# Kernel tuning notes

Measured on AMD Instinct MI355X. Metric: run time of the kernel, lower is better.

Reference implementation:

```python
import jax, jax.numpy as jnp
import numpy as np

NUM_LAYERS = 6
D_MODEL = 768
N_HEADS = 8
D_QKV = D_MODEL // N_HEADS
D_FF = 3072
OUT_DIM = 80
MAX_REL = 100  # relative_positional_distance
NUM_REL = 2 * MAX_REL + 1
LN_EPS = 1e-5


def layer_norm(x, g, b):
    mu = jnp.mean(x, axis=-1, keepdims=True)
    var = jnp.mean((x - mu) ** 2, axis=-1, keepdims=True)
    return (x - mu) / jnp.sqrt(var + LN_EPS) * g + b


def rel_positional_logits(q, emb):
    # q: (B,H,L,dq) (already scaled by 1/sqrt(dq)); emb: (H, 2*MAX_REL+1, dq)
    B, H, L, dq = q.shape
    pad_len = max(L - MAX_REL, 0)
    start = max(MAX_REL - L, 0)
    padded = jnp.pad(emb, ((0, 0), (pad_len, pad_len), (0, 0)))
    used = padded[:, start:start + 2 * L - 1]  # (H, 2L-1, dq)
    logits = jnp.einsum('bhld,hmd->bhlm', q, used)  # (B,H,L,2L-1)
    if L > MAX_REL:
        # mask unreachable relative positions (|rel| beyond table) with -1e8
        mask = jnp.zeros((2 * L - 1,), logits.dtype)
        mask = mask.at[:pad_len].set(-1e8).at[-pad_len:].set(-1e8)
        logits = logits + mask
    # relative -> absolute indexing (fairseq skew trick)
    x = jnp.pad(logits, ((0, 0), (0, 0), (0, 0), (0, 1)))       # (B,H,L,2L)
    x = x.reshape(B, H, L * 2 * L)
    x = jnp.pad(x, ((0, 0), (0, 0), (0, L - 1)))
    x = x.reshape(B, H, L + 1, 2 * L - 1)
    return x[:, :, :L, L - 1:]  # (B,H,L,L)


def self_attention(x, wq, wk, wv, wo, emb):
    # x: (T,B,D); wq/wk/wv: (H,D,dq); wo: (H,dq,D); emb: (H,NUM_REL,dq)
    q = jnp.einsum('tbf,hfa->bhta', x, wq) / (D_QKV ** 0.5)
    k = jnp.einsum('tbf,hfa->bhta', x, wk)
    v = jnp.einsum('tbf,hfa->bhta', x, wv)
    logits = jnp.einsum('bhqa,bhka->bhqk', q, k) + rel_positional_logits(q, emb)
    probs = jax.nn.softmax(logits, axis=-1)
    o = jnp.einsum('bhqk,bhka->bhqa', probs, v)
    return jnp.einsum('bhta,had->tbd', o, wo)


def forward(x, wq, wk, wv, wo, rel_emb, ff1_w, ff1_b, ff2_w, ff2_b,
            ln1_g, ln1_b, ln2_g, ln2_b, wout, bout):
    # x: (B,T,D)
    src = jnp.transpose(x, (1, 0, 2))  # (T,B,D)
    for l in range(NUM_LAYERS):
        attn = self_attention(src, wq[l], wk[l], wv[l], wo[l], rel_emb[l])
        src = layer_norm(src + attn, ln1_g[l], ln1_b[l])
        h = jax.nn.relu(src @ ff1_w[l].T + ff1_b[l])
        ff = h @ ff2_w[l].T + ff2_b[l]
        src = layer_norm(src + ff, ln2_g[l], ln2_b[l])
    out = jnp.transpose(src, (1, 0, 2))  # (B,T,D)
    return out @ wout.T + bout


def setup_inputs() -> dict:
    key = jax.random.key(0)
    ks = jax.random.split(key, 17)
    B, T = 8, 512
    s_d = 1.0 / np.sqrt(D_MODEL)
    s_q = 1.0 / np.sqrt(D_QKV)
    s_f = 1.0 / np.sqrt(D_FF)
    f32 = jnp.float32
    return {
        'x': jax.random.normal(ks[0], (B, T, D_MODEL), f32),
        'wq': jax.random.normal(ks[1], (NUM_LAYERS, N_HEADS, D_MODEL, D_QKV), f32) * s_d,
        'wk': jax.random.normal(ks[2], (NUM_LAYERS, N_HEADS, D_MODEL, D_QKV), f32) * s_d,
        'wv': jax.random.normal(ks[3], (NUM_LAYERS, N_HEADS, D_MODEL, D_QKV), f32) * s_d,
        'wo': jax.random.normal(ks[4], (NUM_LAYERS, N_HEADS, D_QKV, D_MODEL), f32) * s_q,
        'rel_emb': jax.random.normal(ks[5], (NUM_LAYERS, N_HEADS, NUM_REL, D_QKV), f32) * s_q,
        'ff1_w': jax.random.normal(ks[6], (NUM_LAYERS, D_FF, D_MODEL), f32) * s_d,
        'ff1_b': jnp.zeros((NUM_LAYERS, D_FF), f32),
        'ff2_w': jax.random.normal(ks[7], (NUM_LAYERS, D_MODEL, D_FF), f32) * s_f,
        'ff2_b': jnp.zeros((NUM_LAYERS, D_MODEL), f32),
        'ln1_g': jnp.ones((NUM_LAYERS, D_MODEL), f32),
        'ln1_b': jnp.zeros((NUM_LAYERS, D_MODEL), f32),
        'ln2_g': jnp.ones((NUM_LAYERS, D_MODEL), f32),
        'ln2_b': jnp.zeros((NUM_LAYERS, D_MODEL), f32),
        'wout': jax.random.normal(ks[8], (OUT_DIM, D_MODEL), f32) * s_d,
        'bout': jnp.zeros((OUT_DIM,), f32),
    }


def reference(x, wq, wk, wv, wo, rel_emb, ff1_w, ff1_b, ff2_w, ff2_b,
              ln1_g, ln1_b, ln2_g, ln2_b, wout, bout):
    return forward(x, wq, wk, wv, wo, rel_emb, ff1_w, ff1_b, ff2_w, ff2_b,
                   ln1_g, ln1_b, ln2_g, ln2_b, wout, bout)
```

## Files before the change

### kernel.cpp

```cpp
#include <hip/hip_runtime.h>
#include <hip/hip_bf16.h>
#include <math.h>

#define NL   6
#define DM   768
#define NH   8
#define DQ   96
#define DFF  3072
#define BB   8
#define TT   512
#define NTOK (BB*TT)
#define NREL 201
#define WIN  99
#define ODIM 80
#define NQKV 2304
#define RELD 208

typedef __attribute__((ext_vector_type(8))) short v8s;
typedef __attribute__((ext_vector_type(4))) float v4f;

static __device__ __forceinline__ short bf16bits(float x) {
  __hip_bfloat16 h = __float2bfloat16(x);
  return *(short*)&h;
}
static __device__ __forceinline__ unsigned short bf16u(float x) {
  __hip_bfloat16 h = __float2bfloat16(x);
  return *(unsigned short*)&h;
}

__global__ void k_transpose_in(const float* __restrict__ x, float* __restrict__ src,
                               __hip_bfloat16* __restrict__ srcb) {
  int n = blockIdx.x;
  int t = n >> 3, b = n & 7;
  const float* xi = x + ((size_t)b*TT + t)*DM;
  for (int d = threadIdx.x; d < DM; d += blockDim.x) {
    float v = xi[d];
    src[(size_t)n*DM + d] = v;
    srcb[(size_t)n*DM + d] = __float2bfloat16(v);
  }
}

__global__ __launch_bounds__(256)
void k_conv_qkvw(const float* __restrict__ wq, const float* __restrict__ wk,
                 const float* __restrict__ wv, __hip_bfloat16* __restrict__ o) {
  __shared__ float tile[64][33];
  const int ft = blockIdx.x, at = blockIdx.y;
  const int l = blockIdx.z >> 3, h = blockIdx.z & 7;
  const int f0 = ft*64, a0 = at*32;
  const int tx = threadIdx.x & 31, ty = threadIdx.x >> 5;
  const float* srcs[3] = {wq, wk, wv};
  #pragma unroll
  for (int part = 0; part < 3; ++part) {
    const float* s = srcs[part] + (size_t)l*DM*DM + (size_t)h*DM*DQ;
    #pragma unroll
    for (int p = 0; p < 8; ++p)
      tile[ty + 8*p][tx] = s[(size_t)(f0 + ty + 8*p)*DQ + (a0 + tx)];
    __syncthreads();
    const float sc = (part == 0) ? 0.10206207261596577f : 1.f;
    unsigned short* d = (unsigned short*)o + (size_t)l*NQKV*DM + (size_t)(part*DM + h*DQ)*DM;
    #pragma unroll
    for (int p = 0; p < 4; ++p) {
      int a = ty + 8*p;
      int f = 2*tx;
      ushort2 pr = make_ushort2(bf16u(tile[f][a]*sc), bf16u(tile[f+1][a]*sc));
      *(ushort2*)(d + (size_t)(a0 + a)*DM + f0 + f) = pr;
    }
    __syncthreads();
  }
}

__global__ __launch_bounds__(256)
void k_conv_wo(const float* __restrict__ wo, __hip_bfloat16* __restrict__ o) {
  __shared__ float tile[64][33];
  const int rt = blockIdx.x, dt = blockIdx.y, l = blockIdx.z;
  const int r0 = rt*64, d0 = dt*32;
  const int tx = threadIdx.x & 31, ty = threadIdx.x >> 5;
  const float* s = wo + (size_t)l*DM*DM;
  #pragma unroll
  for (int p = 0; p < 8; ++p)
    tile[ty + 8*p][tx] = s[(size_t)(r0 + ty + 8*p)*DM + d0 + tx];
  __syncthreads();
  unsigned short* d = (unsigned short*)o + (size_t)l*DM*DM;
  #pragma unroll
  for (int p = 0; p < 4; ++p) {
    int dd = ty + 8*p;
    int r = 2*tx;
    ushort2 pr = make_ushort2(bf16u(tile[r][dd]), bf16u(tile[r+1][dd]));
    *(ushort2*)(d + (size_t)(d0 + dd)*DM + r0 + r) = pr;
  }
}

__global__ void k_cast(const float* __restrict__ in, __hip_bfloat16* __restrict__ o, size_t n) {
  size_t idx = (size_t)blockIdx.x*256 + threadIdx.x;
  if (idx < n) o[idx] = __float2bfloat16(in[idx]);
}

__global__ void k_conv_wout(const float* __restrict__ wout, __hip_bfloat16* __restrict__ o) {
  int idx = blockIdx.x*256 + threadIdx.x;
  if (idx >= 128*DM) return;
  int n = idx / DM, f = idx % DM;
  o[idx] = __float2bfloat16(n < ODIM ? wout[(size_t)n*DM + f] : 0.f);
}

template<int BM, int BN, int WM, int WN, bool DBUF, bool RELU, bool BF16OUT, bool PERM>
__global__ __launch_bounds__(256)
void k_mfma_gemm(const __hip_bfloat16* __restrict__ A, const __hip_bfloat16* __restrict__ Bt,
                 const float* __restrict__ bias, void* __restrict__ Cv,
                 int K, int Nvalid, int ldc) {
  constexpr int NWN = BN/WN;
  constexpr int FM = WM/16, FN = WN/16;
  constexpr int NB = DBUF ? 2 : 1;
  __shared__ __align__(16) short As[NB][BM*64];
  __shared__ __align__(16) short Bs[NB][BN*64];
  const int tid = threadIdx.x;
  const int m0 = blockIdx.x*BM, n0 = blockIdx.y*BN;
  const int lane = tid & 63, w = tid >> 6;
  const int wm = (w / NWN)*WM, wn = (w % NWN)*WN;
  const int mr = lane & 15, q4 = lane >> 4;
  const short* Ag = (const short*)A;
  const short* Bg = (const short*)Bt;
  const v4f zero = {0.f, 0.f, 0.f, 0.f};
  v4f acc[FM][FN];
  #pragma unroll
  for (int i=0;i<FM;++i)
    #pragma unroll
    for (int j=0;j<FN;++j) acc[i][j] = zero;

  auto stage = [&](int k0, int buf) {
    #pragma unroll
    for (int s = 0; s < (BM*8)/256; ++s) {
      int cid = s*256 + tid;
      int row = cid >> 3;
      int c = (cid & 7) ^ (row & 7);
      __builtin_amdgcn_global_load_lds(
        (const __attribute__((address_space(1))) void*)(Ag + (size_t)(m0+row)*K + k0 + c*8),
        (__attribute__((address_space(3))) void*)(&As[buf][cid*8]), 16, 0, 0);
    }
    #pragma unroll
    for (int s = 0; s < (BN*8)/256; ++s) {
      int cid = s*256 + tid;
      int row = cid >> 3;
      int c = (cid & 7) ^ (row & 7);
      __builtin_amdgcn_global_load_lds(
        (const __attribute__((address_space(1))) void*)(Bg + (size_t)(n0+row)*K + k0 + c*8),
        (__attribute__((address_space(3))) void*)(&Bs[buf][cid*8]), 16, 0, 0);
    }
  };

  auto compute = [&](const short* Ab, const short* Bb) {
    #pragma unroll
    for (int kh = 0; kh < 2; ++kh) {
      int pos = (kh*4 + q4) ^ (mr & 7);
      v8s af[FM], bf[FN];
      #pragma unroll
      for (int ii=0;ii<FM;++ii) af[ii] = *(const v8s*)(Ab + (wm + ii*16 + mr)*64 + pos*8);
      #pragma unroll
      for (int j=0;j<FN;++j) bf[j] = *(const v8s*)(Bb + (wn + j*16 + mr)*64 + pos*8);
      #pragma unroll
      for (int ii=0;ii<FM;++ii)
        #pragma unroll
        for (int j=0;j<FN;++j)
          acc[ii][j] = __builtin_amdgcn_mfma_f32_16x16x32_bf16(af[ii], bf[j], acc[ii][j], 0, 0, 0);
    }
  };

  const int nk = K >> 6;
  if (DBUF) {
    stage(0, 0);
    for (int i = 0; i < nk; ++i) {
      __syncthreads();
      if (i + 1 < nk) stage((i+1)*64, (i+1)&1);
      compute(As[i&1], Bs[i&1]);
    }
  } else {
    for (int i = 0; i < nk; ++i) {
      stage(i*64, 0);
      __syncthreads();
      compute(As[0], Bs[0]);
      __syncthreads();
    }
  }

  #pragma unroll
  for (int j=0;j<FN;++j) {
    int col = n0 + wn + j*16 + mr;
    if (col < Nvalid) {
      float bv = bias ? bias[col] : 0.f;
      #pragma unroll
      for (int i=0;i<FM;++i) {
        #pragma unroll
        for (int r=0;r<4;++r) {
          int m = m0 + wm + i*16 + q4*4 + r;
          float val = acc[i][j][r] + bv;
          if (RELU) val = fmaxf(val, 0.f);
          int row = PERM ? ((m & 7)*TT + (m >> 3)) : m;
          if (BF16OUT) ((__hip_bfloat16*)Cv)[(size_t)row*ldc + col] = __float2bfloat16(val);
          else         ((float*)Cv)[(size_t)row*ldc + col] = val;
        }
      }
    }
  }
}

__global__ __launch_bounds__(256)
void k_rel_gemm(const __hip_bfloat16* __restrict__ qkvb,
                const __hip_bfloat16* __restrict__ embb,
                float* __restrict__ rel) {
  const int e0 = blockIdx.x*64, m0 = blockIdx.y*64, h = blockIdx.z;
  const int tid = threadIdx.x, lane = tid & 63, w = tid >> 6;
  const int l15 = lane & 15, q4 = lane >> 4;
  __shared__ __align__(16) short As[64*104];
  __shared__ __align__(16) short Bs[64*104];
  const short* qg = (const short*)qkvb;
  const short* eg = (const short*)embb;
  {
    int row = tid >> 2;
    const short* sa = qg + (size_t)(m0+row)*NQKV + h*DQ;
    int er = e0 + row; if (er > 200) er = 200;
    const short* sb = eg + ((size_t)h*NREL + er)*DQ;
    short* da = As + row*104;
    short* db = Bs + row*104;
    #pragma unroll
    for (int c = 0; c < 3; ++c) {
      int ch = (tid & 3)*3 + c;
      *(v8s*)(da + ch*8) = *(const v8s*)(sa + ch*8);
      *(v8s*)(db + ch*8) = *(const v8s*)(sb + ch*8);
    }
  }
  __syncthreads();
  const v4f zero = {0.f,0.f,0.f,0.f};
  v4f acc[4] = {zero, zero, zero, zero};
  #pragma unroll
  for (int ks = 0; ks < 3; ++ks) {
    v8s af = *(const v8s*)(As + (w*16 + l15)*104 + ks*32 + q4*8);
    #pragma unroll
    for (int f = 0; f < 4; ++f) {
      v8s bf = *(const v8s*)(Bs + (f*16 + l15)*104 + ks*32 + q4*8);
      acc[f] = __builtin_amdgcn_mfma_f32_16x16x32_bf16(af, bf, acc[f], 0, 0, 0);
    }
  }
  #pragma unroll
  for (int f = 0; f < 4; ++f) {
    int e = e0 + f*16 + l15;
    if (e < 2*WIN + 1) {
      #pragma unroll
      for (int r = 0; r < 4; ++r) {
        int n = m0 + w*16 + q4*4 + r;
        rel[((size_t)h*NTOK + n)*RELD + e] = acc[f][r];
      }
    }
  }
}

__global__ __launch_bounds__(256)
void k_attn_mfma(const __hip_bfloat16* __restrict__ qkvb,
                 const float* __restrict__ rel,
                 __hip_bfloat16* __restrict__ o) {
  const int qt = blockIdx.x, h = blockIdx.y, b = blockIdx.z;
  const int qlo = qt*64;
  const int tid = threadIdx.x, lane = tid & 63, w = tid >> 6;
  const int l15 = lane & 15, q4 = lane >> 4;
  __shared__ __align__(16) short Qs[64*104];
  __shared__ __align__(16) short Ks[64*104];
  __shared__ __align__(16) short Vt[96*72];
  __shared__ __align__(16) short Ps[64*72];
  const short* qg = (const short*)qkvb;

  {
    int row = tid >> 2;
    const short* src = qg + (size_t)((qlo+row)*8 + b)*NQKV + h*DQ;
    short* dst = Qs + row*104;
    #pragma unroll
    for (int c = 0; c < 3; ++c) {
      int ch = (tid & 3)*3 + c;
      *(v8s*)(dst + ch*8) = *(const v8s*)(src + ch*8);
    }
  }

  v4f sacc[5][4];
  const v4f neg = {-1e30f,-1e30f,-1e30f,-1e30f};
  #pragma unroll
  for (int kt=0;kt<5;++kt)
    #pragma unroll
    for (int f=0;f<4;++f) sacc[kt][f] = neg;

  const int i_row0 = qlo + w*16 + q4*4;

  for (int kt = 0; kt < 5; ++kt) {
    int kt0 = qlo + kt*64 - 128;
    if (kt0 + 64 <= 0 || kt0 >= TT) continue;
    {
      int row = tid >> 2;
      int j = kt0 + row; j = j < 0 ? 0 : (j > TT-1 ? TT-1 : j);
      const short* src = qg + (size_t)(j*8 + b)*NQKV + DM + h*DQ;
      short* dst = Ks + row*104;
      #pragma unroll
      for (int c = 0; c < 3; ++c) {
        int ch = (tid & 3)*3 + c;
        *(v8s*)(dst + ch*8) = *(const v8s*)(src + ch*8);
      }
    }
    __syncthreads();
    #pragma unroll
    for (int f = 0; f < 4; ++f) {
      int j = kt0 + f*16 + l15;
      #pragma unroll
      for (int r = 0; r < 4; ++r) {
        int i = i_row0 + r;
        int d = j - i;
        float val = -1e30f;
        if (j >= 0 && j < TT && d >= -WIN && d <= WIN)
          val = rel[((size_t)h*NTOK + i*8 + b)*RELD + d + WIN];
        sacc[kt][f][r] = val;
      }
    }
    #pragma unroll
    for (int ks = 0; ks < 3; ++ks) {
      v8s af = *(const v8s*)(Qs + (w*16 + l15)*104 + ks*32 + q4*8);
      #pragma unroll
      for (int f = 0; f < 4; ++f) {
        v8s bf = *(const v8s*)(Ks + (f*16 + l15)*104 + ks*32 + q4*8);
        sacc[kt][f] = __builtin_amdgcn_mfma_f32_16x16x32_bf16(af, bf, sacc[kt][f], 0, 0, 0);
      }
    }
    __syncthreads();
  }

  float inv[4];
  #pragma unroll
  for (int r = 0; r < 4; ++r) {
    float m = -1e30f;
    #pragma unroll
    for (int kt=0;kt<5;++kt)
      #pragma unroll
      for (int f=0;f<4;++f) m = fmaxf(m, sacc[kt][f][r]);
    #pragma unroll
    for (int off=1; off<16; off<<=1) m = fmaxf(m, __shfl_xor(m, off));
    float l = 0.f;
    #pragma unroll
    for (int kt=0;kt<5;++kt)
      #pragma unroll
      for (int f=0;f<4;++f) {
        float p = __expf(sacc[kt][f][r] - m);
        sacc[kt][f][r] = p; l += p;
      }
    #pragma unroll
    for (int off=1; off<16; off<<=1) l += __shfl_xor(l, off);
    inv[r] = 1.f / l;
  }

  v4f oacc[6];
  const v4f zero = {0.f,0.f,0.f,0.f};
  #pragma unroll
  for (int f=0;f<6;++f) oacc[f] = zero;
  for (int kt = 0; kt < 5; ++kt) {
    int kt0 = qlo + kt*64 - 128;
    if (kt0 + 64 <= 0 || kt0 >= TT) continue;
    #pragma unroll
    for (int f=0;f<4;++f)
      #pragma unroll
      for (int r=0;r<4;++r)
        Ps[(w*16 + q4*4 + r)*72 + f*16 + l15] = bf16bits(sacc[kt][f][r]);
    {
      int j = kt0 + (tid >> 2);
      int jc = j < 0 ? 0 : (j > TT-1 ? TT-1 : j);
      const short* src = qg + (size_t)(jc*8 + b)*NQKV + 2*DM + h*DQ + (tid & 3)*24;
      union { v8s v[3]; short s[24]; } u;
      u.v[0] = *(const v8s*)(src);
      u.v[1] = *(const v8s*)(src + 8);
      u.v[2] = *(const v8s*)(src + 16);
      int a0 = (tid & 3)*24, jl = tid >> 2;
      #pragma unroll
      for (int t=0;t<24;++t) Vt[(a0+t)*72 + jl] = u.s[t];
    }
    __syncthreads();
    #pragma unroll
    for (int ks=0;ks<2;++ks) {
      v8s af = *(const v8s*)(Ps + (w*16 + l15)*72 + ks*32 + q4*8);
      #pragma unroll
      for (int f=0;f<6;++f) {
        v8s bf = *(const v8s*)(Vt + (f*16 + l15)*72 + ks*32 + q4*8);
        oacc[f] = __builtin_amdgcn_mfma_f32_16x16x32_bf16(af, bf, oacc[f], 0, 0, 0);
      }
    }
    __syncthreads();
  }

  #pragma unroll
  for (int f=0;f<6;++f)
    #pragma unroll
    for (int r=0;r<4;++r) {
      int i = i_row0 + r;
      o[(size_t)(i*8 + b)*DM + h*DQ + f*16 + l15] = __float2bfloat16(oacc[f][r] * inv[r]);
    }
}

__global__ __launch_bounds__(256)
void k_ln_residual(float* __restrict__ src, const float* __restrict__ res,
                   const float* __restrict__ g, const float* __restrict__ bta,
                   __hip_bfloat16* __restrict__ srcb) {
  __shared__ float red[4];
  int n = blockIdx.x;
  float x[3];
  float s = 0.f;
  #pragma unroll
  for (int u=0;u<3;++u) {
    int d = u*256 + threadIdx.x;
    x[u] = src[(size_t)n*DM + d] + res[(size_t)n*DM + d];
    s += x[u];
  }
  #pragma unroll
  for (int off=32; off; off>>=1) s += __shfl_xor(s, off);
  if ((threadIdx.x & 63) == 0) red[threadIdx.x>>6] = s;
  __syncthreads();
  float mu = (red[0]+red[1]+red[2]+red[3]) * (1.f/DM);
  __syncthreads();
  float vs = 0.f;
  #pragma unroll
  for (int u=0;u<3;++u) { float dv = x[u]-mu; vs += dv*dv; }
  #pragma unroll
  for (int off=32; off; off>>=1) vs += __shfl_xor(vs, off);
  if ((threadIdx.x & 63) == 0) red[threadIdx.x>>6] = vs;
  __syncthreads();
  float rstd = rsqrtf((red[0]+red[1]+red[2]+red[3])*(1.f/DM) + 1e-5f);
  #pragma unroll
  for (int u=0;u<3;++u) {
    int d = u*256 + threadIdx.x;
    float v = (x[u]-mu)*rstd*g[d] + bta[d];
    src[(size_t)n*DM + d] = v;
    srcb[(size_t)n*DM + d] = __float2bfloat16(v);
  }
}

extern "C" void kernel_launch(void* const* d_in, const int* in_sizes, int n_in,
                              void* d_out, int out_size, void* d_ws, size_t ws_size,
                              hipStream_t stream) {
  const float* x    = (const float*)d_in[0];
  const float* wq   = (const float*)d_in[1];
  const float* wk   = (const float*)d_in[2];
  const float* wv   = (const float*)d_in[3];
  const float* wo   = (const float*)d_in[4];
  const float* remb = (const float*)d_in[5];
  const float* ff1w = (const float*)d_in[6];
  const float* ff1b = (const float*)d_in[7];
  const float* ff2w = (const float*)d_in[8];
  const float* ff2b = (const float*)d_in[9];
  const float* ln1g = (const float*)d_in[10];
  const float* ln1b = (const float*)d_in[11];
  const float* ln2g = (const float*)d_in[12];
  const float* ln2b = (const float*)d_in[13];
  const float* wout = (const float*)d_in[14];
  const float* bout = (const float*)d_in[15];
  float* out = (float*)d_out;

  float* wsp = (float*)d_ws;
  size_t off = 0;
  float* src  = wsp + off;                              off += (size_t)NTOK*DM;
  __hip_bfloat16* srcb  = (__hip_bfloat16*)(wsp + off); off += (size_t)NTOK*DM/2;
  __hip_bfloat16* qkvb  = (__hip_bfloat16*)(wsp + off); off += (size_t)NTOK*NQKV/2;
  float* rel  = wsp + off;                              off += (size_t)NH*NTOK*RELD;
  float* tmp  = wsp + off;                              off += (size_t)NTOK*DM;
  __hip_bfloat16* qkvwbA = (__hip_bfloat16*)(wsp + off); off += (size_t)NL*NQKV*DM/2;
  __hip_bfloat16* wobA   = (__hip_bfloat16*)(wsp + off); off += (size_t)NL*DM*DM/2;
  __hip_bfloat16* ff1wbA = (__hip_bfloat16*)(wsp + off); off += (size_t)NL*DFF*DM/2;
  __hip_bfloat16* ff2wbA = (__hip_bfloat16*)(wsp + off); off += (size_t)NL*DM*DFF/2;
  __hip_bfloat16* woutb  = (__hip_bfloat16*)(wsp + off); off += (size_t)128*DM/2;
  __hip_bfloat16* embbA  = (__hip_bfloat16*)(wsp + off); off += (size_t)NL*NH*NREL*DQ/2 + 64;
  __hip_bfloat16* hb  = (__hip_bfloat16*)qkvb;
  __hip_bfloat16* obb = srcb;
  (void)off; (void)ws_size; (void)in_sizes; (void)n_in; (void)out_size;

  dim3 b256(256);

  k_conv_qkvw<<<dim3(DM/64, DQ/32, NL*NH), b256, 0, stream>>>(wq, wk, wv, qkvwbA);
  k_conv_wo<<<dim3(DM/64, DM/32, NL), b256, 0, stream>>>(wo, wobA);
  k_cast<<<dim3(((size_t)NL*DFF*DM+255)/256), b256, 0, stream>>>(ff1w, ff1wbA, (size_t)NL*DFF*DM);
  k_cast<<<dim3(((size_t)NL*DM*DFF+255)/256), b256, 0, stream>>>(ff2w, ff2wbA, (size_t)NL*DM*DFF);
  k_cast<<<dim3(((size_t)NL*NH*NREL*DQ+255)/256), b256, 0, stream>>>(remb, embbA, (size_t)NL*NH*NREL*DQ);
  k_conv_wout<<<dim3((128*DM+255)/256), b256, 0, stream>>>(wout, woutb);

  k_transpose_in<<<dim3(NTOK), b256, 0, stream>>>(x, src, srcb);

  for (int l = 0; l < NL; ++l) {
    __hip_bfloat16* qkvwb = qkvwbA + (size_t)l*NQKV*DM;
    __hip_bfloat16* wob   = wobA   + (size_t)l*DM*DM;
    __hip_bfloat16* ff1wb = ff1wbA + (size_t)l*DFF*DM;
    __hip_bfloat16* ff2wb = ff2wbA + (size_t)l*DM*DFF;
    __hip_bfloat16* embb  = embbA  + (size_t)l*NH*NREL*DQ;

    k_mfma_gemm<128,128,64,64,false,false,true,false><<<dim3(NTOK/128, NQKV/128), b256, 0, stream>>>(
        srcb, qkvwb, nullptr, qkvb, DM, NQKV, NQKV);

    k_rel_gemm<<<dim3(4, NTOK/64, NH), b256, 0, stream>>>(qkvb, embb, rel);

    k_attn_mfma<<<dim3(TT/64, NH, BB), b256, 0, stream>>>(qkvb, rel, obb);

    k_mfma_gemm<64,64,32,32,true,false,false,false><<<dim3(NTOK/64, DM/64), b256, 0, stream>>>(
        obb, wob, nullptr, tmp, DM, DM, DM);
    k_ln_residual<<<dim3(NTOK), b256, 0, stream>>>(src, tmp, ln1g + (size_t)l*DM, ln1b + (size_t)l*DM, srcb);

    k_mfma_gemm<128,128,64,64,false,true,true,false><<<dim3(NTOK/128, DFF/128), b256, 0, stream>>>(
        srcb, ff1wb, ff1b + (size_t)l*DFF, hb, DM, DFF, DFF);
    k_mfma_gemm<64,64,32,32,true,false,false,false><<<dim3(NTOK/64, DM/64), b256, 0, stream>>>(
        hb, ff2wb, ff2b + (size_t)l*DM, tmp, DFF, DM, DM);
    k_ln_residual<<<dim3(NTOK), b256, 0, stream>>>(src, tmp, ln2g + (size_t)l*DM, ln2b + (size_t)l*DM, srcb);
  }

  k_mfma_gemm<64,128,64,32,true,false,false,true><<<dim3(NTOK/64, 1), b256, 0, stream>>>(
      srcb, woutb, bout, out, DM, ODIM, ODIM);
}
```

Before: 1.147 ms.

## Use 32x32x16 MFMA GEMM with double buffering for all layer projections

Adds a new GEMM kernel built on the 32x32x16 bf16 MFMA instruction, with double-buffered LDS staging. It is used for the QKV, output-projection, FF1 and FF2 GEMMs. Double buffering becomes unconditional in the existing 16x16 kernel, which now serves only the final output projection. The FF2 tile changes to 128x64. The larger MFMA shape is meant to cut LDS fragment loads per flop and improve MFMA throughput, at the cost of more accumulator registers and LDS per block, which may lower occupancy.

```diff
diff --git a/kernel.cpp b/kernel.cpp
--- a/kernel.cpp
+++ b/kernel.cpp
@@ -18,6 +18,7 @@
 
 typedef __attribute__((ext_vector_type(8))) short v8s;
 typedef __attribute__((ext_vector_type(4))) float v4f;
+typedef __attribute__((ext_vector_type(16))) float v16f;
 
 static __device__ __forceinline__ short bf16bits(float x) {
   __hip_bfloat16 h = __float2bfloat16(x);
@@ -102,16 +103,106 @@
   o[idx] = __float2bfloat16(n < ODIM ? wout[(size_t)n*DM + f] : 0.f);
 }
 
-template<int BM, int BN, int WM, int WN, bool DBUF, bool RELU, bool BF16OUT, bool PERM>
+template<int BM, int BN, int WM, int WN, bool RELU, bool BF16OUT>
+__global__ __launch_bounds__(256)
+void k_gemm32(const __hip_bfloat16* __restrict__ A, const __hip_bfloat16* __restrict__ Bt,
+              const float* __restrict__ bias, void* __restrict__ Cv,
+              int K, int ldc) {
+  constexpr int NWN = BN/WN;
+  constexpr int FM = WM/32, FN = WN/32;
+  __shared__ __align__(16) short As[2][BM*64];
+  __shared__ __align__(16) short Bs[2][BN*64];
+  const int tid = threadIdx.x;
+  const int m0 = blockIdx.x*BM, n0 = blockIdx.y*BN;
+  const int lane = tid & 63, w = tid >> 6;
+  const int wm = (w / NWN)*WM, wn = (w % NWN)*WN;
+  const int r31 = lane & 31, h = lane >> 5;
+  const short* Ag = (const short*)A;
+  const short* Bg = (const short*)Bt;
+  v16f acc[FM][FN];
+  #pragma unroll
+  for (int i=0;i<FM;++i)
+    #pragma unroll
+    for (int j=0;j<FN;++j)
+      #pragma unroll
+      for (int r=0;r<16;++r) acc[i][j][r] = 0.f;
+
+  auto stage = [&](int k0, int buf) {
+    #pragma unroll
+    for (int s = 0; s < (BM*8)/256; ++s) {
+      int cid = s*256 + tid;
+      int row = cid >> 3;
+      int c = (cid & 7) ^ (row & 7);
+      __builtin_amdgcn_global_load_lds(
+        (const __attribute__((address_space(1))) void*)(Ag + (size_t)(m0+row)*K + k0 + c*8),
+        (__attribute__((address_space(3))) void*)(&As[buf][cid*8]), 16, 0, 0);
+    }
+    #pragma unroll
+    for (int s = 0; s < (BN*8)/256; ++s) {
+      int cid = s*256 + tid;
+      int row = cid >> 3;
+      int c = (cid & 7) ^ (row & 7);
+      __builtin_amdgcn_global_load_lds(
+        (const __attribute__((address_space(1))) void*)(Bg + (size_t)(n0+row)*K + k0 + c*8),
+        (__attribute__((address_space(3))) void*)(&Bs[buf][cid*8]), 16, 0, 0);
+    }
+  };
+
+  const int nk = K >> 6;
+  stage(0, 0);
+  for (int it = 0; it < nk; ++it) {
+    __syncthreads();
+    if (it + 1 < nk) stage((it+1)*64, (it+1)&1);
+    const short* Ab = As[it&1];
+    const short* Bb = Bs[it&1];
+    #pragma unroll
+    for (int ks = 0; ks < 4; ++ks) {
+      v8s af[FM], bf[FN];
+      #pragma unroll
+      for (int i=0;i<FM;++i) {
+        int r = wm + i*32 + r31;
+        af[i] = *(const v8s*)(Ab + r*64 + (((ks<<1)|h) ^ (r&7))*8);
+      }
+      #pragma unroll
+      for (int j=0;j<FN;++j) {
+        int r = wn + j*32 + r31;
+        bf[j] = *(const v8s*)(Bb + r*64 + (((ks<<1)|h) ^ (r&7))*8);
+      }
+      #pragma unroll
+      for (int i=0;i<FM;++i)
+        #pragma unroll
+        for (int j=0;j<FN;++j)
+          acc[i][j] = __builtin_amdgcn_mfma_f32_32x32x16_bf16(af[i], bf[j], acc[i][j], 0, 0, 0);
+    }
+  }
+
+  #pragma unroll
+  for (int j=0;j<FN;++j) {
+    int col = n0 + wn + j*32 + r31;
+    float bv = bias ? bias[col] : 0.f;
+    #pragma unroll
+    for (int i=0;i<FM;++i) {
+      #pragma unroll
+      for (int r=0;r<16;++r) {
+        int m = m0 + wm + i*32 + (r&3) + 8*(r>>2) + 4*h;
+        float val = acc[i][j][r] + bv;
+        if (RELU) val = fmaxf(val, 0.f);
+        if (BF16OUT) ((__hip_bfloat16*)Cv)[(size_t)m*ldc + col] = __float2bfloat16(val);
+        else         ((float*)Cv)[(size_t)m*ldc + col] = val;
+      }
+    }
+  }
+}
+
+template<int BM, int BN, int WM, int WN, bool RELU, bool BF16OUT, bool PERM>
 __global__ __launch_bounds__(256)
 void k_mfma_gemm(const __hip_bfloat16* __restrict__ A, const __hip_bfloat16* __restrict__ Bt,
                  const float* __restrict__ bias, void* __restrict__ Cv,
                  int K, int Nvalid, int ldc) {
   constexpr int NWN = BN/WN;
   constexpr int FM = WM/16, FN = WN/16;
-  constexpr int NB = DBUF ? 2 : 1;
-  __shared__ __align__(16) short As[NB][BM*64];
-  __shared__ __align__(16) short Bs[NB][BN*64];
+  __shared__ __align__(16) short As[2][BM*64];
+  __shared__ __align__(16) short Bs[2][BN*64];
   const int tid = threadIdx.x;
   const int m0 = blockIdx.x*BM, n0 = blockIdx.y*BN;
   const int lane = tid & 63, w = tid >> 6;
@@ -147,7 +238,13 @@
     }
   };
 
-  auto compute = [&](const short* Ab, const short* Bb) {
+  const int nk = K >> 6;
+  stage(0, 0);
+  for (int it = 0; it < nk; ++it) {
+    __syncthreads();
+    if (it + 1 < nk) stage((it+1)*64, (it+1)&1);
+    const short* Ab = As[it&1];
+    const short* Bb = Bs[it&1];
     #pragma unroll
     for (int kh = 0; kh < 2; ++kh) {
       int pos = (kh*4 + q4) ^ (mr & 7);
@@ -161,23 +258,6 @@
         #pragma unroll
         for (int j=0;j<FN;++j)
           acc[ii][j] = __builtin_amdgcn_mfma_f32_16x16x32_bf16(af[ii], bf[j], acc[ii][j], 0, 0, 0);
-    }
-  };
-
-  const int nk = K >> 6;
-  if (DBUF) {
-    stage(0, 0);
-    for (int i = 0; i < nk; ++i) {
-      __syncthreads();
-      if (i + 1 < nk) stage((i+1)*64, (i+1)&1);
-      compute(As[i&1], Bs[i&1]);
-    }
-  } else {
-    for (int i = 0; i < nk; ++i) {
-      stage(i*64, 0);
-      __syncthreads();
-      compute(As[0], Bs[0]);
-      __syncthreads();
     }
   }
 
@@ -488,24 +568,24 @@
     __hip_bfloat16* ff2wb = ff2wbA + (size_t)l*DM*DFF;
     __hip_bfloat16* embb  = embbA  + (size_t)l*NH*NREL*DQ;
 
-    k_mfma_gemm<128,128,64,64,false,false,true,false><<<dim3(NTOK/128, NQKV/128), b256, 0, stream>>>(
-        srcb, qkvwb, nullptr, qkvb, DM, NQKV, NQKV);
+    k_gemm32<128,128,64,64,false,true><<<dim3(NTOK/128, NQKV/128), b256, 0, stream>>>(
+        srcb, qkvwb, nullptr, qkvb, DM, NQKV);
 
     k_rel_gemm<<<dim3(4, NTOK/64, NH), b256, 0, stream>>>(qkvb, embb, rel);
 
     k_attn_mfma<<<dim3(TT/64, NH, BB), b256, 0, stream>>>(qkvb, rel, obb);
 
-    k_mfma_gemm<64,64,32,32,true,false,false,false><<<dim3(NTOK/64, DM/64), b256, 0, stream>>>(
-        obb, wob, nullptr, tmp, DM, DM, DM);
+    k_gemm32<64,64,32,32,false,false><<<dim3(NTOK/64, DM/64), b256, 0, stream>>>(
+        obb, wob, nullptr, tmp, DM, DM);
     k_ln_residual<<<dim3(NTOK), b256, 0, stream>>>(src, tmp, ln1g + (size_t)l*DM, ln1b + (size_t)l*DM, srcb);
 
-    k_mfma_gemm<128,128,64,64,false,true,true,false><<<dim3(NTOK/128, DFF/128), b256, 0, stream>>>(
-        srcb, ff1wb, ff1b + (size_t)l*DFF, hb, DM, DFF, DFF);
-    k_mfma_gemm<64,64,32,32,true,false,false,false><<<dim3(NTOK/64, DM/64), b256, 0, stream>>>(
-        hb, ff2wb, ff2b + (size_t)l*DM, tmp, DFF, DM, DM);
+    k_gemm32<128,128,64,64,true,true><<<dim3(NTOK/128, DFF/128), b256, 0, stream>>>(
+        srcb, ff1wb, ff1b + (size_t)l*DFF, hb, DM, DFF);
+    k_gemm32<128,64,64,32,false,false><<<dim3(NTOK/128, DM/64), b256, 0, stream>>>(
+        hb, ff2wb, ff2b + (size_t)l*DM, tmp, DFF, DM);
     k_ln_residual<<<dim3(NTOK), b256, 0, stream>>>(src, tmp, ln2g + (size_t)l*DM, ln2b + (size_t)l*DM, srcb);
   }
 
-  k_mfma_gemm<64,128,64,32,true,false,false,true><<<dim3(NTOK/64, 1), b256, 0, stream>>>(
+  k_mfma_gemm<64,128,64,32,false,false,true><<<dim3(NTOK/64, 1), b256, 0, stream>>>(
       srcb, woutb, bout, out, DM, ODIM, ODIM);
 }
```

New measurement: 1.274 ms. 11.1% more time.
